# Kernel optimization log

Hardware: AMD Instinct MI355X
Metric: run time of the kernel (lower is better)

The kernel has to match this reference:

```python
import jax, jax.numpy as jnp
import numpy as np

B, C = 32768, 1000
EPS = 1e-6

def setup_inputs() -> dict:
    key = jax.random.key(0)
    k1, k2 = jax.random.split(key)
    # p_tar / p_vlm are probability distributions over C classes
    p_tar = jax.nn.softmax(jax.random.normal(k1, (B, C), dtype=jnp.float32), axis=1)
    p_vlm = jax.nn.softmax(jax.random.normal(k2, (B, C), dtype=jnp.float32), axis=1)
    alpha = jnp.array([0.99], dtype=jnp.float32)  # EMA momentum
    memory_bank = jnp.full((C, C), 1.0 / C, dtype=jnp.float32)  # __init__ state
    return {"p_tar": p_tar, "p_vlm": p_vlm, "alpha": alpha, "memory_bank": memory_bank}

def _uncertainty(p):
    return -p * jnp.log(p + EPS)

def reference(p_tar, p_vlm, alpha, memory_bank):
    n_classes = memory_bank.shape[0]
    norm = 1.0 / jnp.sqrt(jnp.float32(n_classes))
    # --- class_prototype_atten (uses PRE-update memory bank, as in torch) ---
    atten = jax.nn.softmax(jnp.matmul(p_tar, memory_bank.T) * norm, axis=1)  # [B, C]
    p_tar_new = jnp.matmul(atten, memory_bank)  # [B, C]
    # --- update_membank: vectorized per-class masked-mean EMA ---
    y_tar = jnp.argmax(p_tar, axis=1)
    y_vlm = jnp.argmax(p_vlm, axis=1)
    agree = y_tar == y_vlm
    # non-agreeing rows dumped into extra segment n_classes
    seg = jnp.where(agree, y_tar, n_classes)
    sums = jax.ops.segment_sum(p_tar, seg, num_segments=n_classes + 1)[:n_classes]  # [C, C]
    counts = jax.ops.segment_sum(agree.astype(p_tar.dtype), seg, num_segments=n_classes + 1)[:n_classes]  # [C]
    has = counts > 0
    mean = sums / jnp.where(has, counts, 1.0)[:, None]
    a = alpha.reshape(())
    bank_new = jnp.where(has[:, None], a * memory_bank + (1.0 - a) * mean, memory_bank)
    # --- uncertainty_mixing ---
    eu_tar = jnp.exp(-_uncertainty(p_tar_new))
    eu_vlm = jnp.exp(-_uncertainty(p_vlm))
    p_mix = (eu_tar * p_tar_new + eu_vlm * p_vlm) / (eu_tar + eu_vlm)
    return p_mix, bank_new
```

## Files before the change

### kernel.cpp

```cpp
#include <hip/hip_runtime.h>
#include <hip/hip_bf16.h>
#include <cstdint>
#include <cstddef>

#define NROWS 32768
#define NCLS  1000
#define KP    1024
#define NCH   32

typedef unsigned short u16;
typedef __bf16 bf16x8 __attribute__((ext_vector_type(8)));
typedef float  f32x4  __attribute__((ext_vector_type(4)));


__device__ __forceinline__ void gld_lds16(const u16* g, u16* l) {
  __builtin_amdgcn_global_load_lds(
      (const __attribute__((address_space(1))) unsigned int*)g,
      (__attribute__((address_space(3))) unsigned int*)l, 16, 0, 0);
}

__global__ __launch_bounds__(128)
void prep4_bank(const float* __restrict__ bank,
                __hip_bfloat16* __restrict__ M4,
                __hip_bfloat16* __restrict__ MT4) {
  __shared__ float tile[32][33];
  const int tx = blockIdx.x;
  const int ty = blockIdx.y;
  const int t  = threadIdx.x;
  {
    const int r = t >> 2, c0 = (t & 3) * 8;
    const int gj = ty * 32 + r;
    #pragma unroll
    for (int j = 0; j < 8; ++j) {
      const int gk = tx * 32 + c0 + j;
      tile[r][c0 + j] = (gj < NCLS && gk < NCLS) ? bank[gj * NCLS + gk] : 0.0f;
    }
  }
  __syncthreads();
  const int w = t >> 6, lane = t & 63, lr = lane & 15, qq = lane >> 4;
  if (w == 0) {
    #pragma unroll
    for (int s = 0; s < 2; ++s) {
      bf16x8 o;
      #pragma unroll
      for (int j = 0; j < 8; ++j) o[j] = (__bf16)tile[s * 16 + lr][qq * 8 + j];
      *(bf16x8*)((u16*)M4 + ((size_t)(ty * 2 + s) * NCH + tx) * 512 + lane * 8) = o;
    }
  } else {
    #pragma unroll
    for (int s = 0; s < 2; ++s) {
      bf16x8 o;
      #pragma unroll
      for (int j = 0; j < 8; ++j) o[j] = (__bf16)tile[qq * 8 + j][s * 16 + lr];
      *(bf16x8*)((u16*)MT4 + ((size_t)(tx * 2 + s) * NCH + ty) * 512 + lane * 8) = o;
    }
  }
}

__global__ __launch_bounds__(256)
void rows4_kernel(const float* __restrict__ p_tar, const float* __restrict__ p_vlm,
                  __hip_bfloat16* __restrict__ A4,
                  float* __restrict__ sums, float* __restrict__ counts) {
  __shared__ float sT[4][16]; __shared__ int siT[4][16];
  __shared__ float sV[4][16]; __shared__ int siV[4][16];
  const int w = threadIdx.x >> 6, lane = threadIdx.x & 63;
  const int lr = lane & 15, q = lane >> 4;
  const int panel = blockIdx.x;
  const int row   = panel * 16 + lr;
  const float* tr = p_tar + (size_t)row * NCLS;
  const float* vr = p_vlm + (size_t)row * NCLS;
  u16* a4 = (u16*)A4 + (size_t)panel * NCH * 512 + lane * 8;

  float bvT = -1.0f; int biT = 0;
  float bvV = -1.0f; int biV = 0;
  for (int c = w * 8; c < w * 8 + 8; ++c) {
    const int k0 = c * 32 + q * 8;
    float v[8];
    if (k0 < NCLS) {
      float4 x = *(const float4*)(tr + k0);
      float4 y = *(const float4*)(tr + k0 + 4);
      v[0] = x.x; v[1] = x.y; v[2] = x.z; v[3] = x.w;
      v[4] = y.x; v[5] = y.y; v[6] = y.z; v[7] = y.w;
    } else {
      #pragma unroll
      for (int j = 0; j < 8; ++j) v[j] = 0.0f;
    }
    bf16x8 o;
    #pragma unroll
    for (int j = 0; j < 8; ++j) {
      o[j] = (__bf16)v[j];
      if (v[j] > bvT) { bvT = v[j]; biT = k0 + j; }
    }
    *(bf16x8*)(a4 + (size_t)c * 512) = o;
    if (k0 < NCLS) {
      float4 x = *(const float4*)(vr + k0);
      float4 y = *(const float4*)(vr + k0 + 4);
      float u[8] = {x.x, x.y, x.z, x.w, y.x, y.y, y.z, y.w};
      #pragma unroll
      for (int j = 0; j < 8; ++j)
        if (u[j] > bvV) { bvV = u[j]; biV = k0 + j; }
    }
  }
  #pragma unroll
  for (int d = 16; d < 64; d <<= 1) {
    float ov = __shfl_xor(bvT, d); int oi = __shfl_xor(biT, d);
    if (ov > bvT || (ov == bvT && oi < biT)) { bvT = ov; biT = oi; }
    float ov2 = __shfl_xor(bvV, d); int oi2 = __shfl_xor(biV, d);
    if (ov2 > bvV || (ov2 == bvV && oi2 < biV)) { bvV = ov2; biV = oi2; }
  }
  if (q == 0) { sT[w][lr] = bvT; siT[w][lr] = biT; sV[w][lr] = bvV; siV[w][lr] = biV; }
  __syncthreads();
  float cT = sT[0][lr]; int ciT = siT[0][lr];
  float cV = sV[0][lr]; int ciV = siV[0][lr];
  #pragma unroll
  for (int ww = 1; ww < 4; ++ww) {
    float v1 = sT[ww][lr]; if (v1 > cT) { cT = v1; ciT = siT[ww][lr]; }
    float v2 = sV[ww][lr]; if (v2 > cV) { cV = v2; ciV = siV[ww][lr]; }
  }
  if (w == 0) {
    const int ag = (ciT == ciV) ? 1 : 0;
    for (int rr = 0; rr < 16; ++rr) {
      const int agr = __shfl(ag, rr);
      if (agr) {
        const int cls = __shfl(ciT, rr);
        const float* trr = p_tar + (size_t)(panel * 16 + rr) * NCLS;
        for (int k = lane; k < NCLS; k += 64)
          atomicAdd(&sums[(size_t)cls * NCLS + k], trr[k]);
        if (lane == 0) atomicAdd(&counts[cls], 1.0f);
      }
    }
  }
}

template <int WHICH>
__global__ __launch_bounds__(256, 3)
void gemm4(const u16* __restrict__ A4, const u16* __restrict__ B4,
           __hip_bfloat16* __restrict__ E4out, float* __restrict__ rowsum,
           const float* __restrict__ p_vlm, float* __restrict__ mix_out) {
  __shared__ u16 SH[6][4096];
  const int tid  = threadIdx.x;
  const int w    = tid >> 6;
  const int lane = tid & 63;
  const int lr   = lane & 15;
  const int q    = lane >> 4;
  const int L    = blockIdx.x;
  const int xcd  = L & 7;
  const int jj   = L >> 3;
  const int bm   = xcd * 32 + (jj >> 3);
  const int bn   = jj & 7;
  const int wm   = w >> 1;
  const int wn   = w & 1;

  f32x4 acc[4][4] = {};

  const u16* ga0 = A4 + ((size_t)(bm * 8 + 2 * w) * NCH) * 512 + lane * 8;
  const u16* ga1 = ga0 + (size_t)NCH * 512;
  const u16* gb0 = B4 + ((size_t)(bn * 8 + 2 * w) * NCH) * 512 + lane * 8;
  const u16* gb1 = gb0 + (size_t)NCH * 512;

  #define STAGE4(kk, b)                                            \
    do {                                                           \
      const size_t ko = (size_t)(kk) * 512;                        \
      gld_lds16(ga0 + ko, &SH[(b)][(2 * w + 0) * 512]);            \
      gld_lds16(ga1 + ko, &SH[(b)][(2 * w + 1) * 512]);            \
      gld_lds16(gb0 + ko, &SH[3 + (b)][(2 * w + 0) * 512]);        \
      gld_lds16(gb1 + ko, &SH[3 + (b)][(2 * w + 1) * 512]);        \
    } while (0)

  STAGE4(0, 0);
  STAGE4(1, 1);

  int cur = 0;
  for (int i = 0; i < NCH; ++i) {
    if (i < NCH - 1) {
      asm volatile("s_waitcnt vmcnt(4)" ::: "memory");
    } else {
      asm volatile("s_waitcnt vmcnt(0)" ::: "memory");
    }
    __builtin_amdgcn_s_barrier();
    asm volatile("" ::: "memory");
    if (i + 2 < NCH) {
      int b2 = cur + 2; if (b2 >= 3) b2 -= 3;
      STAGE4(i + 2, b2);
    }
    bf16x8 af[4], bfr[4];
    #pragma unroll
    for (int t = 0; t < 4; ++t) {
      af[t]  = *(const bf16x8*)(&SH[cur][(wm * 4 + t) * 512 + lane * 8]);
      bfr[t] = *(const bf16x8*)(&SH[3 + cur][(wn * 4 + t) * 512 + lane * 8]);
    }
    #pragma unroll
    for (int mt = 0; mt < 4; ++mt)
      #pragma unroll
      for (int nt = 0; nt < 4; ++nt)
        acc[mt][nt] = __builtin_amdgcn_mfma_f32_16x16x32_bf16(af[mt], bfr[nt], acc[mt][nt], 0, 0, 0);
    cur = (cur == 2) ? 0 : cur + 1;
  }
  #undef STAGE4

  const float NORM = 0.03162277660168379f;
  if (WHICH == 1) {
    __syncthreads();
    u16* ep = &SH[w][0];
    #pragma unroll
    for (int mt = 0; mt < 4; ++mt) {
      float psum[4] = {0.f, 0.f, 0.f, 0.f};
      #pragma unroll
      for (int nt = 0; nt < 4; ++nt) {
        const int gn = bn * 128 + wn * 64 + nt * 16 + lr;
        const int cc = nt >> 1;
        const int q2 = (nt & 1) * 2 + (lr >> 3);
        const int jj2 = lr & 7;
        #pragma unroll
        for (int r = 0; r < 4; ++r) {
          float e = (gn < NCLS) ? __expf(acc[mt][nt][r] * NORM) : 0.0f;
          psum[r] += e;
          __hip_bfloat16 h = __float2bfloat16(e);
          ep[(mt * 2 + cc) * 512 + (q2 * 16 + q * 4 + r) * 8 + jj2] = *(u16*)&h;
        }
      }
      #pragma unroll
      for (int r = 0; r < 4; ++r) {
        float s = psum[r];
        s += __shfl_xor(s, 1); s += __shfl_xor(s, 2);
        s += __shfl_xor(s, 4); s += __shfl_xor(s, 8);
        if (lr == 0) atomicAdd(&rowsum[bm * 128 + wm * 64 + mt * 16 + q * 4 + r], s);
      }
    }
    #pragma unroll
    for (int ch = 0; ch < 8; ++ch) {
      const int mt = ch >> 1, cc = ch & 1;
      bf16x8 v = *(const bf16x8*)(&ep[ch * 512 + lane * 8]);
      const size_t Rg = bm * 8 + wm * 4 + mt;
      const size_t cg = bn * 4 + wn * 2 + cc;
      *(bf16x8*)((u16*)E4out + (Rg * NCH + cg) * 512 + lane * 8) = v;
    }
  } else {
    #pragma unroll
    for (int mt = 0; mt < 4; ++mt) {
      #pragma unroll
      for (int r = 0; r < 4; ++r) {
        const int gm = bm * 128 + wm * 64 + mt * 16 + q * 4 + r;
        const float inv = 1.0f / rowsum[gm];
        #pragma unroll
        for (int nt = 0; nt < 4; ++nt) {
          const int gn = bn * 128 + wn * 64 + nt * 16 + lr;
          if (gn < NCLS) {
            float pt = acc[mt][nt][r] * inv;
            float pv = p_vlm[(size_t)gm * NCLS + gn];
            float lt = pt * __logf(pt + 1e-6f);
            float lv = pv * __logf(pv + 1e-6f);
            float rr = __expf(lv - lt);
            mix_out[(size_t)gm * NCLS + gn] = (pt + rr * pv) / (1.0f + rr);
          }
        }
      }
    }
  }
}

__global__ __launch_bounds__(256)
void bank_update(const float* __restrict__ bank, const float* __restrict__ sums,
                 const float* __restrict__ counts, const float* __restrict__ alpha,
                 float* __restrict__ out) {
  const int idx = blockIdx.x * 256 + threadIdx.x;
  if (idx >= NCLS * NCLS) return;
  const int r = idx / NCLS;
  const float cnt = counts[r];
  const float bv  = bank[idx];
  const float a   = alpha[0];
  out[idx] = (cnt > 0.0f) ? a * bv + (1.0f - a) * (sums[idx] / cnt) : bv;
}

extern "C" void kernel_launch(void* const* d_in, const int* in_sizes, int n_in,
                              void* d_out, int out_size, void* d_ws, size_t ws_size,
                              hipStream_t stream) {
  const float* p_tar = (const float*)d_in[0];
  const float* p_vlm = (const float*)d_in[1];
  const float* alpha = (const float*)d_in[2];
  const float* bank  = (const float*)d_in[3];
  float* out_mix  = (float*)d_out;
  float* out_bank = (float*)d_out + (size_t)NROWS * NCLS;

  char* w = (char*)d_ws;
  __hip_bfloat16* A4  = (__hip_bfloat16*)w; w += (size_t)NROWS * KP * 2;
  __hip_bfloat16* E4  = (__hip_bfloat16*)w; w += (size_t)NROWS * KP * 2;
  __hip_bfloat16* M4  = (__hip_bfloat16*)w; w += (size_t)KP * KP * 2;
  __hip_bfloat16* MT4 = (__hip_bfloat16*)w; w += (size_t)KP * KP * 2;
  float* sums   = (float*)w;                w += (size_t)NCLS * NCLS * 4;
  float* counts = (float*)w;                w += 1024 * 4;
  float* rs     = (float*)w;                w += (size_t)NROWS * 4;

  hipMemsetAsync(sums, 0, (size_t)NCLS * NCLS * 4 + 1024 * 4 + (size_t)NROWS * 4, stream);

  prep4_bank<<<dim3(32, 32), 128, 0, stream>>>(bank, M4, MT4);
  rows4_kernel<<<NROWS / 16, 256, 0, stream>>>(p_tar, p_vlm, A4, sums, counts);
  gemm4<1><<<2048, 256, 0, stream>>>(
      (const u16*)A4, (const u16*)M4, E4, rs, nullptr, nullptr);
  gemm4<2><<<2048, 256, 0, stream>>>(
      (const u16*)E4, (const u16*)MT4, nullptr, rs, p_vlm, out_mix);
  bank_update<<<(NCLS * NCLS + 255) / 256, 256, 0, stream>>>(bank, sums, counts, alpha, out_bank);
}
```

Measured before the change: 565.2 us.

## Load GEMM fragments directly from global memory instead of LDS-staged pipeline

Removes the triple-buffered global_load_lds staging and barriers from the gemm4 main loop; each wave now reads its A and B bf16x8 fragments straight from global memory, relying on L2/L1 for reuse across waves. LDS shrinks to the epilogue scratch only, and launch bounds raise the occupancy target from 3 to 4 blocks per CU. This trades explicit shared-memory reuse and async prefetch for fewer barriers and higher occupancy, at the risk of more redundant global/L2 traffic and exposed load latency.

```diff
diff --git a/kernel.cpp b/kernel.cpp
--- a/kernel.cpp
+++ b/kernel.cpp
@@ -12,12 +12,6 @@
 typedef __bf16 bf16x8 __attribute__((ext_vector_type(8)));
 typedef float  f32x4  __attribute__((ext_vector_type(4)));
 
-
-__device__ __forceinline__ void gld_lds16(const u16* g, u16* l) {
-  __builtin_amdgcn_global_load_lds(
-      (const __attribute__((address_space(1))) unsigned int*)g,
-      (__attribute__((address_space(3))) unsigned int*)l, 16, 0, 0);
-}
 
 __global__ __launch_bounds__(128)
 void prep4_bank(const float* __restrict__ bank,
@@ -133,11 +127,11 @@
 }
 
 template <int WHICH>
-__global__ __launch_bounds__(256, 3)
+__global__ __launch_bounds__(256, 4)
 void gemm4(const u16* __restrict__ A4, const u16* __restrict__ B4,
            __hip_bfloat16* __restrict__ E4out, float* __restrict__ rowsum,
            const float* __restrict__ p_vlm, float* __restrict__ mix_out) {
-  __shared__ u16 SH[6][4096];
+  __shared__ u16 SH[4][4096];
   const int tid  = threadIdx.x;
   const int w    = tid >> 6;
   const int lane = tid & 63;
@@ -153,54 +147,31 @@
 
   f32x4 acc[4][4] = {};
 
-  const u16* ga0 = A4 + ((size_t)(bm * 8 + 2 * w) * NCH) * 512 + lane * 8;
-  const u16* ga1 = ga0 + (size_t)NCH * 512;
-  const u16* gb0 = B4 + ((size_t)(bn * 8 + 2 * w) * NCH) * 512 + lane * 8;
-  const u16* gb1 = gb0 + (size_t)NCH * 512;
-
-  #define STAGE4(kk, b)                                            \
-    do {                                                           \
-      const size_t ko = (size_t)(kk) * 512;                        \
-      gld_lds16(ga0 + ko, &SH[(b)][(2 * w + 0) * 512]);            \
-      gld_lds16(ga1 + ko, &SH[(b)][(2 * w + 1) * 512]);            \
-      gld_lds16(gb0 + ko, &SH[3 + (b)][(2 * w + 0) * 512]);        \
-      gld_lds16(gb1 + ko, &SH[3 + (b)][(2 * w + 1) * 512]);        \
-    } while (0)
-
-  STAGE4(0, 0);
-  STAGE4(1, 1);
-
-  int cur = 0;
+  const u16* ga[4];
+  const u16* gb[4];
+  #pragma unroll
+  for (int t = 0; t < 4; ++t) {
+    ga[t] = A4 + ((size_t)(bm * 8 + wm * 4 + t) * NCH) * 512 + lane * 8;
+    gb[t] = B4 + ((size_t)(bn * 8 + wn * 4 + t) * NCH) * 512 + lane * 8;
+  }
+
+  #pragma unroll 2
   for (int i = 0; i < NCH; ++i) {
-    if (i < NCH - 1) {
-      asm volatile("s_waitcnt vmcnt(4)" ::: "memory");
-    } else {
-      asm volatile("s_waitcnt vmcnt(0)" ::: "memory");
-    }
-    __builtin_amdgcn_s_barrier();
-    asm volatile("" ::: "memory");
-    if (i + 2 < NCH) {
-      int b2 = cur + 2; if (b2 >= 3) b2 -= 3;
-      STAGE4(i + 2, b2);
-    }
+    const size_t kc = (size_t)i * 512;
     bf16x8 af[4], bfr[4];
     #pragma unroll
-    for (int t = 0; t < 4; ++t) {
-      af[t]  = *(const bf16x8*)(&SH[cur][(wm * 4 + t) * 512 + lane * 8]);
-      bfr[t] = *(const bf16x8*)(&SH[3 + cur][(wn * 4 + t) * 512 + lane * 8]);
-    }
+    for (int t = 0; t < 4; ++t) af[t]  = *(const bf16x8*)(ga[t] + kc);
+    #pragma unroll
+    for (int t = 0; t < 4; ++t) bfr[t] = *(const bf16x8*)(gb[t] + kc);
     #pragma unroll
     for (int mt = 0; mt < 4; ++mt)
       #pragma unroll
       for (int nt = 0; nt < 4; ++nt)
         acc[mt][nt] = __builtin_amdgcn_mfma_f32_16x16x32_bf16(af[mt], bfr[nt], acc[mt][nt], 0, 0, 0);
-    cur = (cur == 2) ? 0 : cur + 1;
-  }
-  #undef STAGE4
+  }
 
   const float NORM = 0.03162277660168379f;
   if (WHICH == 1) {
-    __syncthreads();
     u16* ep = &SH[w][0];
     #pragma unroll
     for (int mt = 0; mt < 4; ++mt) {
```

After: 649.7 us. 15.0% more time.
